# Performance work log

Hardware: AMD Instinct MI355X
Metric: run time of the kernel (lower is better)

Reference implementation:

```python
import jax, jax.numpy as jnp
import numpy as np

MARGIN = 0.2
NEG_INF = -1e30
POS_INF = 1e30


def setup_inputs() -> dict:
    key = jax.random.key(0)
    k1, k2 = jax.random.split(key)
    B, D = 8192, 128
    im = jax.random.normal(k1, (B, D), dtype=jnp.float32)
    ids = jax.random.randint(k2, (B,), 0, 512, dtype=jnp.int64)
    return {"im": im, "ids": ids}


def reference(im, ids):
    # scores[i, j] = <im_i, im_j>, with the diagonal zeroed (as in the original,
    # which sets scores[j][j] = 0 before mining). Note the positive set includes
    # the anchor itself, so min over positives includes the zeroed diagonal.
    B = im.shape[0]
    scores = im @ im.T                      # [B, B]
    scores = scores * (1.0 - jnp.eye(B, dtype=scores.dtype))
    pos_mask = ids[:, None] == ids[None, :]  # same id (includes self)
    neg_mask = ~pos_mask
    max_neg = jnp.max(jnp.where(neg_mask, scores, NEG_INF), axis=1)  # hardest negative per anchor
    min_pos = jnp.min(jnp.where(pos_mask, scores, POS_INF), axis=1)  # hardest positive per anchor
    cost = jnp.sum(jnp.maximum(MARGIN + max_neg - min_pos, 0.0))
    return cost
```

## Files before the change

kernel.cpp:

```cpp
#include <hip/hip_runtime.h>
#include <hip/hip_bf16.h>

#define MARGIN  0.2f
#define NEG_INF -1e30f
#define POS_INF 1e30f

#define B_SZ 8192
#define D_SZ 128

typedef __bf16 bf16x8 __attribute__((ext_vector_type(8)));
typedef __bf16 bf16x4 __attribute__((ext_vector_type(4)));
typedef float  f32x4  __attribute__((ext_vector_type(4)));

__global__ __launch_bounds__(256) void k_convert(const float* __restrict__ in,
                                                 __bf16* __restrict__ out, int n) {
    int i = (blockIdx.x * 256 + threadIdx.x) * 4;
    if (i < n) {
        float4 v = *reinterpret_cast<const float4*>(in + i);
        bf16x4 o;
        o[0] = (__bf16)v.x; o[1] = (__bf16)v.y; o[2] = (__bf16)v.z; o[3] = (__bf16)v.w;
        *reinterpret_cast<bf16x4*>(out + i) = o;
    }
}

__global__ __launch_bounds__(256) void k_mine(const __bf16* __restrict__ imb,
                                              const int* __restrict__ ids,
                                              float* __restrict__ wsmax,
                                              float* __restrict__ wsmin) {
    const int rb  = blockIdx.x;
    const int cs  = blockIdx.y;
    const int tid = threadIdx.x;
    const int w    = tid >> 6;
    const int lane = tid & 63;
    const int quad = lane >> 4;
    const int lr   = lane & 15;

    __shared__ int   ids_s[1024];
    __shared__ float red_mx[4][64];
    __shared__ float red_mn[4][64];

    const int colsplit0 = cs * 1024;
    reinterpret_cast<int4*>(ids_s)[tid] =
        reinterpret_cast<const int4*>(ids + colsplit0)[tid];

    const int rowbase = rb * 64;

    bf16x8 afrag[4][4];
    #pragma unroll
    for (int s = 0; s < 4; ++s) {
        const __bf16* p = imb + (size_t)(rowbase + s * 16 + lr) * D_SZ + quad * 8;
        #pragma unroll
        for (int kf = 0; kf < 4; ++kf)
            afrag[s][kf] = *reinterpret_cast<const bf16x8*>(p + kf * 32);
    }

    int   rowv[4][4];
    int   rid [4][4];
    float mxn [4][4];
    float mnp [4][4];
    #pragma unroll
    for (int s = 0; s < 4; ++s)
        #pragma unroll
        for (int r = 0; r < 4; ++r) {
            rowv[s][r] = rowbase + s * 16 + quad * 4 + r;
            rid [s][r] = ids[rowv[s][r]];
            mxn [s][r] = NEG_INF;
            mnp [s][r] = POS_INF;
        }

    __syncthreads();

    #pragma unroll 1
    for (int t = 0; t < 16; ++t) {
        const int tile    = w * 16 + t;
        const int colbase = colsplit0 + tile * 16;
        const int colv    = colbase + lr;
        const int cid     = ids_s[tile * 16 + lr];

        bf16x8 bfrag[4];
        const __bf16* q = imb + (size_t)colv * D_SZ + quad * 8;
        #pragma unroll
        for (int kf = 0; kf < 4; ++kf)
            bfrag[kf] = *reinterpret_cast<const bf16x8*>(q + kf * 32);

        #pragma unroll
        for (int s = 0; s < 4; ++s) {
            f32x4 acc = {0.f, 0.f, 0.f, 0.f};
            #pragma unroll
            for (int kf = 0; kf < 4; ++kf)
                acc = __builtin_amdgcn_mfma_f32_16x16x32_bf16(afrag[s][kf], bfrag[kf], acc, 0, 0, 0);
            #pragma unroll
            for (int r = 0; r < 4; ++r) {
                float sv   = acc[r];
                bool  same = (rid[s][r] == cid);
                bool  diag = (rowv[s][r] == colv);
                mxn[s][r] = fmaxf(mxn[s][r], same ? NEG_INF : sv);
                mnp[s][r] = fminf(mnp[s][r], (same && !diag) ? sv : POS_INF);
            }
        }
    }

    #pragma unroll
    for (int s = 0; s < 4; ++s)
        #pragma unroll
        for (int r = 0; r < 4; ++r) {
            float mx = mxn[s][r];
            float mn = mnp[s][r];
            #pragma unroll
            for (int m = 1; m < 16; m <<= 1) {
                mx = fmaxf(mx, __shfl_xor(mx, m, 64));
                mn = fminf(mn, __shfl_xor(mn, m, 64));
            }
            if (lr == 0) {
                int rl = s * 16 + quad * 4 + r;
                red_mx[w][rl] = mx;
                red_mn[w][rl] = mn;
            }
        }
    __syncthreads();

    if (tid < 64) {
        float mx = red_mx[0][tid];
        float mn = red_mn[0][tid];
        #pragma unroll
        for (int ww = 1; ww < 4; ++ww) {
            mx = fmaxf(mx, red_mx[ww][tid]);
            mn = fminf(mn, red_mn[ww][tid]);
        }
        wsmax[cs * B_SZ + rowbase + tid] = mx;
        wsmin[cs * B_SZ + rowbase + tid] = mn;
    }
}

__global__ __launch_bounds__(256) void k_final(const float* __restrict__ wsmax,
                                               const float* __restrict__ wsmin,
                                               float* __restrict__ out) {
    int r = blockIdx.x * 256 + threadIdx.x;
    float mx = NEG_INF;
    float mn = 0.0f;
    #pragma unroll
    for (int cs = 0; cs < 8; ++cs) {
        mx = fmaxf(mx, wsmax[cs * B_SZ + r]);
        mn = fminf(mn, wsmin[cs * B_SZ + r]);
    }
    float cost = fmaxf(MARGIN + mx - mn, 0.0f);
    #pragma unroll
    for (int m = 1; m < 64; m <<= 1)
        cost += __shfl_xor(cost, m, 64);
    __shared__ float part[4];
    int lane = threadIdx.x & 63, w = threadIdx.x >> 6;
    if (lane == 0) part[w] = cost;
    __syncthreads();
    if (threadIdx.x == 0)
        atomicAdd(out, part[0] + part[1] + part[2] + part[3]);
}

extern "C" void kernel_launch(void* const* d_in, const int* in_sizes, int n_in,
                              void* d_out, int out_size, void* d_ws, size_t ws_size,
                              hipStream_t stream) {
    const float* im  = (const float*)d_in[0];
    const int*   ids = (const int*)d_in[1];
    float*       out = (float*)d_out;

    __bf16* imb   = (__bf16*)d_ws;
    float*  wsmax = (float*)((char*)d_ws + (size_t)B_SZ * D_SZ * 2);
    float*  wsmin = wsmax + 8 * B_SZ;

    hipMemsetAsync(d_out, 0, sizeof(float), stream);

    k_convert<<<(B_SZ * D_SZ) / (256 * 4), 256, 0, stream>>>(im, imb, B_SZ * D_SZ);
    k_mine<<<dim3(128, 8), 256, 0, stream>>>(imb, ids, wsmax, wsmin);
    k_final<<<B_SZ / 256, 256, 0, stream>>>(wsmax, wsmin, out);
}
```

Measured before the change: 115.8 us.

## Share column tiles across waves, double-buffer B fragments, drop diagonal check

Restructures the mining kernel so all four waves in a block handle different 64-row groups but sweep the same 256-column strip. This lets them share B fragments through cache, and the grid becomes 32x32 blocks. B fragments and column ids are prefetched one tile ahead with register double-buffering, and the LDS id staging and block reduction are removed. Partials are written per column strip in row-major order, and the final kernel reads them with vector loads. The diagonal exclusion is dropped because the zeroed diagonal is covered by the final min starting at 0. Register pressure and the larger partial buffer are the trade-offs.

```diff
diff --git a/kernel.cpp b/kernel.cpp
--- a/kernel.cpp
+++ b/kernel.cpp
@@ -7,43 +7,36 @@
 
 #define B_SZ 8192
 #define D_SZ 128
+#define CS   32
+#define RBS  32
 
 typedef __bf16 bf16x8 __attribute__((ext_vector_type(8)));
-typedef __bf16 bf16x4 __attribute__((ext_vector_type(4)));
 typedef float  f32x4  __attribute__((ext_vector_type(4)));
 
 __global__ __launch_bounds__(256) void k_convert(const float* __restrict__ in,
-                                                 __bf16* __restrict__ out, int n) {
-    int i = (blockIdx.x * 256 + threadIdx.x) * 4;
-    if (i < n) {
-        float4 v = *reinterpret_cast<const float4*>(in + i);
-        bf16x4 o;
-        o[0] = (__bf16)v.x; o[1] = (__bf16)v.y; o[2] = (__bf16)v.z; o[3] = (__bf16)v.w;
-        *reinterpret_cast<bf16x4*>(out + i) = o;
-    }
+                                                 __bf16* __restrict__ out) {
+    int i = (blockIdx.x * 256 + threadIdx.x) * 8;
+    float4 v0 = *reinterpret_cast<const float4*>(in + i);
+    float4 v1 = *reinterpret_cast<const float4*>(in + i + 4);
+    bf16x8 o;
+    o[0] = (__bf16)v0.x; o[1] = (__bf16)v0.y; o[2] = (__bf16)v0.z; o[3] = (__bf16)v0.w;
+    o[4] = (__bf16)v1.x; o[5] = (__bf16)v1.y; o[6] = (__bf16)v1.z; o[7] = (__bf16)v1.w;
+    *reinterpret_cast<bf16x8*>(out + i) = o;
 }
 
 __global__ __launch_bounds__(256) void k_mine(const __bf16* __restrict__ imb,
                                               const int* __restrict__ ids,
                                               float* __restrict__ wsmax,
                                               float* __restrict__ wsmin) {
-    const int rb  = blockIdx.x;
-    const int cs  = blockIdx.y;
-    const int tid = threadIdx.x;
-    const int w    = tid >> 6;
-    const int lane = tid & 63;
+    const int rb   = blockIdx.x;
+    const int cs   = blockIdx.y;
+    const int w    = threadIdx.x >> 6;
+    const int lane = threadIdx.x & 63;
     const int quad = lane >> 4;
     const int lr   = lane & 15;
 
-    __shared__ int   ids_s[1024];
-    __shared__ float red_mx[4][64];
-    __shared__ float red_mn[4][64];
-
-    const int colsplit0 = cs * 1024;
-    reinterpret_cast<int4*>(ids_s)[tid] =
-        reinterpret_cast<const int4*>(ids + colsplit0)[tid];
-
-    const int rowbase = rb * 64;
+    const int rowbase = rb * 256 + w * 64;
+    const int col0    = cs * 256;
 
     bf16x8 afrag[4][4];
     #pragma unroll
@@ -54,48 +47,51 @@
             afrag[s][kf] = *reinterpret_cast<const bf16x8*>(p + kf * 32);
     }
 
-    int   rowv[4][4];
-    int   rid [4][4];
-    float mxn [4][4];
-    float mnp [4][4];
+    int   rid[4][4];
+    float mxn[4][4], mnp[4][4];
     #pragma unroll
     for (int s = 0; s < 4; ++s)
         #pragma unroll
         for (int r = 0; r < 4; ++r) {
-            rowv[s][r] = rowbase + s * 16 + quad * 4 + r;
-            rid [s][r] = ids[rowv[s][r]];
-            mxn [s][r] = NEG_INF;
-            mnp [s][r] = POS_INF;
+            rid[s][r] = ids[rowbase + s * 16 + quad * 4 + r];
+            mxn[s][r] = NEG_INF;
+            mnp[s][r] = POS_INF;
         }
 
-    __syncthreads();
+    const __bf16* bbase = imb + (size_t)col0 * D_SZ;
 
-    #pragma unroll 1
-    for (int t = 0; t < 16; ++t) {
-        const int tile    = w * 16 + t;
-        const int colbase = colsplit0 + tile * 16;
-        const int colv    = colbase + lr;
-        const int cid     = ids_s[tile * 16 + lr];
-
-        bf16x8 bfrag[4];
-        const __bf16* q = imb + (size_t)colv * D_SZ + quad * 8;
+    bf16x8 bbuf[2][4];
+    int    cidb[2];
+    {
+        const __bf16* q = bbase + (size_t)lr * D_SZ + quad * 8;
         #pragma unroll
         for (int kf = 0; kf < 4; ++kf)
-            bfrag[kf] = *reinterpret_cast<const bf16x8*>(q + kf * 32);
+            bbuf[0][kf] = *reinterpret_cast<const bf16x8*>(q + kf * 32);
+        cidb[0] = ids[col0 + lr];
+    }
 
+    #pragma unroll
+    for (int t = 0; t < 16; ++t) {
+        if (t + 1 < 16) {
+            const __bf16* q = bbase + (size_t)((t + 1) * 16 + lr) * D_SZ + quad * 8;
+            #pragma unroll
+            for (int kf = 0; kf < 4; ++kf)
+                bbuf[(t + 1) & 1][kf] = *reinterpret_cast<const bf16x8*>(q + kf * 32);
+            cidb[(t + 1) & 1] = ids[col0 + (t + 1) * 16 + lr];
+        }
+        const int cid = cidb[t & 1];
         #pragma unroll
         for (int s = 0; s < 4; ++s) {
             f32x4 acc = {0.f, 0.f, 0.f, 0.f};
             #pragma unroll
             for (int kf = 0; kf < 4; ++kf)
-                acc = __builtin_amdgcn_mfma_f32_16x16x32_bf16(afrag[s][kf], bfrag[kf], acc, 0, 0, 0);
+                acc = __builtin_amdgcn_mfma_f32_16x16x32_bf16(afrag[s][kf], bbuf[t & 1][kf], acc, 0, 0, 0);
             #pragma unroll
             for (int r = 0; r < 4; ++r) {
                 float sv   = acc[r];
                 bool  same = (rid[s][r] == cid);
-                bool  diag = (rowv[s][r] == colv);
                 mxn[s][r] = fmaxf(mxn[s][r], same ? NEG_INF : sv);
-                mnp[s][r] = fminf(mnp[s][r], (same && !diag) ? sv : POS_INF);
+                mnp[s][r] = fminf(mnp[s][r], same ? sv : POS_INF);
             }
         }
     }
@@ -112,24 +108,11 @@
                 mn = fminf(mn, __shfl_xor(mn, m, 64));
             }
             if (lr == 0) {
-                int rl = s * 16 + quad * 4 + r;
-                red_mx[w][rl] = mx;
-                red_mn[w][rl] = mn;
+                int row = rowbase + s * 16 + quad * 4 + r;
+                wsmax[(size_t)row * CS + cs] = mx;
+                wsmin[(size_t)row * CS + cs] = mn;
             }
         }
-    __syncthreads();
-
-    if (tid < 64) {
-        float mx = red_mx[0][tid];
-        float mn = red_mn[0][tid];
-        #pragma unroll
-        for (int ww = 1; ww < 4; ++ww) {
-            mx = fmaxf(mx, red_mx[ww][tid]);
-            mn = fminf(mn, red_mn[ww][tid]);
-        }
-        wsmax[cs * B_SZ + rowbase + tid] = mx;
-        wsmin[cs * B_SZ + rowbase + tid] = mn;
-    }
 }
 
 __global__ __launch_bounds__(256) void k_final(const float* __restrict__ wsmax,
@@ -139,17 +122,18 @@
     float mx = NEG_INF;
     float mn = 0.0f;
     #pragma unroll
-    for (int cs = 0; cs < 8; ++cs) {
-        mx = fmaxf(mx, wsmax[cs * B_SZ + r]);
-        mn = fminf(mn, wsmin[cs * B_SZ + r]);
+    for (int c = 0; c < CS; c += 4) {
+        f32x4 vx = *reinterpret_cast<const f32x4*>(wsmax + (size_t)r * CS + c);
+        f32x4 vn = *reinterpret_cast<const f32x4*>(wsmin + (size_t)r * CS + c);
+        mx = fmaxf(mx, fmaxf(fmaxf(vx[0], vx[1]), fmaxf(vx[2], vx[3])));
+        mn = fminf(mn, fminf(fminf(vn[0], vn[1]), fminf(vn[2], vn[3])));
     }
     float cost = fmaxf(MARGIN + mx - mn, 0.0f);
     #pragma unroll
     for (int m = 1; m < 64; m <<= 1)
         cost += __shfl_xor(cost, m, 64);
     __shared__ float part[4];
-    int lane = threadIdx.x & 63, w = threadIdx.x >> 6;
-    if (lane == 0) part[w] = cost;
+    if ((threadIdx.x & 63) == 0) part[threadIdx.x >> 6] = cost;
     __syncthreads();
     if (threadIdx.x == 0)
         atomicAdd(out, part[0] + part[1] + part[2] + part[3]);
@@ -164,11 +148,11 @@
 
     __bf16* imb   = (__bf16*)d_ws;
     float*  wsmax = (float*)((char*)d_ws + (size_t)B_SZ * D_SZ * 2);
-    float*  wsmin = wsmax + 8 * B_SZ;
+    float*  wsmin = wsmax + (size_t)B_SZ * CS;
 
     hipMemsetAsync(d_out, 0, sizeof(float), stream);
 
-    k_convert<<<(B_SZ * D_SZ) / (256 * 4), 256, 0, stream>>>(im, imb, B_SZ * D_SZ);
-    k_mine<<<dim3(128, 8), 256, 0, stream>>>(imb, ids, wsmax, wsmin);
+    k_convert<<<(B_SZ * D_SZ) / (256 * 8), 256, 0, stream>>>(im, imb);
+    k_mine<<<dim3(RBS, CS), 256, 0, stream>>>(imb, ids, wsmax, wsmin);
     k_final<<<B_SZ / 256, 256, 0, stream>>>(wsmax, wsmin, out);
 }
```

New measurement: 126.0 us. +8.8%, slower.
